# Kernel optimization log

Hardware: AMD Instinct MI355X
Metric: run time of the kernel (lower is better)

The kernel has to match this reference:

```python
import jax, jax.numpy as jnp
import numpy as np

EMBED_DIM = 512
NUM_HEADS = 8
HEAD_DIM = EMBED_DIM // NUM_HEADS


def setup_inputs() -> dict:
    key = jax.random.key(0)
    ks = jax.random.split(key, 5)
    B, N, D = 2, 4096, EMBED_DIM
    s_in = 1.0 / np.sqrt(D)
    x = jax.random.normal(ks[0], (B, N, D), dtype=jnp.float32)
    qkv_w = jax.random.uniform(ks[1], (3 * D, D), dtype=jnp.float32, minval=-s_in, maxval=s_in)
    qkv_b = jax.random.uniform(ks[2], (3 * D,), dtype=jnp.float32, minval=-s_in, maxval=s_in)
    out_w = jax.random.uniform(ks[3], (D, D), dtype=jnp.float32, minval=-s_in, maxval=s_in)
    out_b = jax.random.uniform(ks[4], (D,), dtype=jnp.float32, minval=-s_in, maxval=s_in)
    return {"x": x, "qkv_w": qkv_w, "qkv_b": qkv_b, "out_w": out_w, "out_b": out_b}


def reference(x, qkv_w, qkv_b, out_w, out_b):
    B, N, D = x.shape
    H, Hd = NUM_HEADS, HEAD_DIM
    # qkv projection: [B,N,3D] -> [3,B,H,N,Hd]
    qkv = x @ qkv_w.T + qkv_b
    qkv = qkv.reshape(B, N, 3, H, Hd).transpose(2, 0, 3, 1, 4)
    q, k, v = qkv[0], qkv[1], qkv[2]
    scale = 1.0 / jnp.sqrt(jnp.asarray(Hd, dtype=x.dtype))
    scores = jnp.einsum("bhnd,bhmd->bhnm", q, k) * scale  # [B,H,N,N]
    weights = jax.nn.softmax(scores, axis=-1)
    out = jnp.einsum("bhnm,bhmd->bhnd", weights, v)  # [B,H,N,Hd]
    out = out.transpose(0, 2, 1, 3).reshape(B, N, D)
    return out @ out_w.T + out_b
```

## Files before the change

### kernel.cpp

```cpp
#include <hip/hip_runtime.h>

typedef __attribute__((ext_vector_type(8))) short short8;
typedef __attribute__((ext_vector_type(4))) float f32x4;
typedef __attribute__((ext_vector_type(16))) float f32x16;
typedef unsigned short u16;
typedef unsigned int u32;

#define SCQ 0.18033688011112042f

__device__ __forceinline__ u16 f2b(float f) {
  unsigned u = __builtin_bit_cast(unsigned, f);
  u += 0x7FFFu + ((u >> 16) & 1u);
  return (u16)(u >> 16);
}

__device__ __forceinline__ u32 cvtpk(float a, float b) {
  u32 r;
  asm("v_cvt_pk_bf16_f32 %0, %1, %2" : "=v"(r) : "v"(a), "v"(b));
  return r;
}

__global__ __launch_bounds__(256) void convert_k(
    const float* __restrict__ x, const float* __restrict__ w1, const float* __restrict__ w2,
    u16* __restrict__ xb, u16* __restrict__ w1b, u16* __restrict__ w2b) {
  const int NXv = (8192 * 512) / 4;
  const int NW1v = (1536 * 512) / 4;
  const int NW2v = (512 * 512) / 4;
  int i = blockIdx.x * 256 + threadIdx.x;
  const float4* src;
  u16* dst;
  int j;
  float scale = 1.0f;
  if (i < NXv) {
    src = (const float4*)x; dst = xb; j = i;
  } else if (i < NXv + NW1v) {
    j = i - NXv; src = (const float4*)w1; dst = w1b;
    if (j < (512 * 512) / 4) scale = SCQ;
  } else {
    j = i - NXv - NW1v;
    if (j >= NW2v) return;
    src = (const float4*)w2; dst = w2b;
  }
  float4 v = src[j];
  ushort4 o;
  o.x = f2b(v.x * scale); o.y = f2b(v.y * scale);
  o.z = f2b(v.z * scale); o.w = f2b(v.w * scale);
  *reinterpret_cast<ushort4*>(dst + (size_t)j * 4) = o;
}

__global__ __launch_bounds__(256) void qkv_gemm(
    const u16* __restrict__ Ab, const u16* __restrict__ Bw, const float* __restrict__ bias,
    u16* __restrict__ Qd, u16* __restrict__ Kd, u16* __restrict__ Vtd) {
  const int m0 = blockIdx.x * 128, n0 = blockIdx.y * 64;
  const int tid = threadIdx.x, wave = tid >> 6, lane = tid & 63;
  const int g = lane >> 4, lr = lane & 15;
  const int wm = (wave >> 1) * 64, wn = (wave & 1) * 32;
  __shared__ alignas(16) u16 Al[128][72];
  __shared__ alignas(16) u16 Bl[64][72];

  f32x4 acc[4][2];
#pragma unroll
  for (int mf = 0; mf < 4; ++mf)
#pragma unroll
    for (int nf = 0; nf < 2; ++nf)
#pragma unroll
      for (int r = 0; r < 4; ++r) acc[mf][nf][r] = 0.0f;

  const int rr = tid >> 3, cc = tid & 7;
  for (int k0 = 0; k0 < 512; k0 += 64) {
    __syncthreads();
#pragma unroll
    for (int it = 0; it < 4; ++it)
      *reinterpret_cast<short8*>(&Al[rr + it * 32][cc * 8]) =
          *reinterpret_cast<const short8*>(Ab + (size_t)(m0 + rr + it * 32) * 512 + k0 + cc * 8);
#pragma unroll
    for (int it = 0; it < 2; ++it)
      *reinterpret_cast<short8*>(&Bl[rr + it * 32][cc * 8]) =
          *reinterpret_cast<const short8*>(Bw + (size_t)(n0 + rr + it * 32) * 512 + k0 + cc * 8);
    __syncthreads();
#pragma unroll
    for (int kb = 0; kb < 2; ++kb) {
      short8 bf[2], af[4];
#pragma unroll
      for (int nf = 0; nf < 2; ++nf)
        bf[nf] = *reinterpret_cast<const short8*>(&Bl[wn + nf * 16 + lr][kb * 32 + g * 8]);
#pragma unroll
      for (int mf = 0; mf < 4; ++mf)
        af[mf] = *reinterpret_cast<const short8*>(&Al[wm + mf * 16 + lr][kb * 32 + g * 8]);
#pragma unroll
      for (int mf = 0; mf < 4; ++mf)
#pragma unroll
        for (int nf = 0; nf < 2; ++nf)
          acc[mf][nf] = __builtin_amdgcn_mfma_f32_16x16x32_bf16(af[mf], bf[nf], acc[mf][nf], 0, 0, 0);
    }
  }
#pragma unroll
  for (int mf = 0; mf < 4; ++mf)
#pragma unroll
    for (int nf = 0; nf < 2; ++nf)
#pragma unroll
      for (int r = 0; r < 4; ++r) {
        int row = m0 + wm + mf * 16 + g * 4 + r;
        int col = n0 + wn + nf * 16 + lr;
        float bv = bias[col];
        if (col < 512) bv *= SCQ;
        u16 val = f2b(acc[mf][nf][r] + bv);
        int which = col >> 9, dcol = col & 511;
        int h = dcol >> 6, hd = dcol & 63;
        int b = row >> 12, n = row & 4095;
        size_t hb = (size_t)(b * 8 + h);
        if (which == 0)      Qd[(hb * 4096 + n) * 64 + hd] = val;
        else if (which == 1) Kd[(hb * 4096 + n) * 64 + hd] = val;
        else                 Vtd[(hb * 64 + hd) * 4096 + n] = val;
      }
}

__global__ __launch_bounds__(256, 2) void attn2(
    const u16* __restrict__ Qd, const u16* __restrict__ Kd, const u16* __restrict__ Vtd,
    float* __restrict__ Op, float* __restrict__ Lp) {
  int f = blockIdx.x + (blockIdx.y << 4) + (blockIdx.z << 8);
  int xcd = f & 7, slot = f >> 3;
  int bh = (xcd << 1) + (slot >> 5);
  int rem = slot & 31;
  int half = rem >> 4;
  int qb = rem & 15;

  const int tid = threadIdx.x, wave = tid >> 6, lane = tid & 63;
  const int hi = lane >> 5, lq = lane & 31;

  const u16* Qh = Qd + (size_t)bh * (4096 * 64);
  const u16* Kh = Kd + (size_t)bh * (4096 * 64);
  const u16* Vh = Vtd + (size_t)bh * (64 * 4096);
  float* Oh = Op + (size_t)half * (8192 * 512);
  float* Lh = Lp + (size_t)half * (16 * 4096);

  __shared__ alignas(16) u16 Kl[2][64 * 64];

  const int qrow_base = qb * 256 + wave * 64;

  short8 qf[2][4];
#pragma unroll
  for (int qt = 0; qt < 2; ++qt)
#pragma unroll
    for (int s = 0; s < 4; ++s)
      qf[qt][s] = *reinterpret_cast<const short8*>(
          Qh + (size_t)(qrow_base + qt * 32 + lq) * 64 + s * 16 + hi * 8);

  f32x16 acc[2][2];
#pragma unroll
  for (int qt = 0; qt < 2; ++qt)
#pragma unroll
    for (int dt = 0; dt < 2; ++dt)
#pragma unroll
      for (int i = 0; i < 16; ++i) acc[qt][dt][i] = 0.0f;

  float lrun[2] = {0.0f, 0.0f};

  const int kv0 = half * 2048;
  const int g0 = tid, g1 = tid + 256;
  const int sr0 = g0 >> 3, sc0 = g0 & 7;
  const int sr1 = g1 >> 3, sc1 = g1 & 7;

  {
    short8 t0 = *reinterpret_cast<const short8*>(Kh + (size_t)(kv0 + sr0) * 64 + sc0 * 8);
    short8 t1 = *reinterpret_cast<const short8*>(Kh + (size_t)(kv0 + sr1) * 64 + sc1 * 8);
    *reinterpret_cast<short8*>(&Kl[0][sr0 * 64 + ((sc0 ^ (sr0 & 7)) << 3)]) = t0;
    *reinterpret_cast<short8*>(&Kl[0][sr1 * 64 + ((sc1 ^ (sr1 & 7)) << 3)]) = t1;
  }
  __syncthreads();

#pragma unroll 1
  for (int kt = 0; kt < 32; ++kt) {
    const int cur = kt & 1;
    const int kbase = kv0 + kt * 64;
    short8 t0, t1;
    const bool pf = (kt + 1 < 32);
    if (pf) {
      t0 = *reinterpret_cast<const short8*>(Kh + (size_t)(kbase + 64 + sr0) * 64 + sc0 * 8);
      t1 = *reinterpret_cast<const short8*>(Kh + (size_t)(kbase + 64 + sr1) * 64 + sc1 * 8);
    }

    f32x16 st[2][2];
#pragma unroll
    for (int qt = 0; qt < 2; ++qt)
#pragma unroll
      for (int krt = 0; krt < 2; ++krt)
#pragma unroll
        for (int i = 0; i < 16; ++i) st[qt][krt][i] = 0.0f;

#pragma unroll
    for (int s = 0; s < 4; ++s) {
      const int ch = ((2 * s + hi) ^ (lq & 7)) << 3;
      short8 kf0 = *reinterpret_cast<const short8*>(&Kl[cur][lq * 64 + ch]);
      short8 kf1 = *reinterpret_cast<const short8*>(&Kl[cur][(32 + lq) * 64 + ch]);
      st[0][0] = __builtin_amdgcn_mfma_f32_32x32x16_bf16(kf0, qf[0][s], st[0][0], 0, 0, 0);
      st[0][1] = __builtin_amdgcn_mfma_f32_32x32x16_bf16(kf1, qf[0][s], st[0][1], 0, 0, 0);
      st[1][0] = __builtin_amdgcn_mfma_f32_32x32x16_bf16(kf0, qf[1][s], st[1][0], 0, 0, 0);
      st[1][1] = __builtin_amdgcn_mfma_f32_32x32x16_bf16(kf1, qf[1][s], st[1][1], 0, 0, 0);
    }

    short8 vf[4][2];
#pragma unroll
    for (int ks = 0; ks < 4; ++ks)
#pragma unroll
      for (int dt = 0; dt < 2; ++dt)
        vf[ks][dt] = *reinterpret_cast<const short8*>(
            Vh + (size_t)(dt * 32 + lq) * 4096 + kbase + ks * 16 + hi * 8);

    short8 pb[2][4];
#pragma unroll
    for (int qt = 0; qt < 2; ++qt) {
      float p[32];
#pragma unroll
      for (int i = 0; i < 16; ++i) p[i] = exp2f(st[qt][0][i]);
#pragma unroll
      for (int i = 0; i < 16; ++i) p[16 + i] = exp2f(st[qt][1][i]);
      float a0 = 0.f, a1 = 0.f, a2 = 0.f, a3 = 0.f;
#pragma unroll
      for (int i = 0; i < 32; i += 4) {
        a0 += p[i]; a1 += p[i + 1]; a2 += p[i + 2]; a3 += p[i + 3];
      }
      lrun[qt] += (a0 + a1) + (a2 + a3);
#pragma unroll
      for (int ks = 0; ks < 4; ++ks) {
        u32 wa = cvtpk(p[8 * ks + 0], p[8 * ks + 1]);
        u32 wb = cvtpk(p[8 * ks + 4], p[8 * ks + 5]);
        u32 wc = cvtpk(p[8 * ks + 2], p[8 * ks + 3]);
        u32 wd = cvtpk(p[8 * ks + 6], p[8 * ks + 7]);
        asm volatile("v_permlane32_swap_b32 %0, %1" : "+v"(wa), "+v"(wb));
        asm volatile("v_permlane32_swap_b32 %0, %1" : "+v"(wc), "+v"(wd));
        int4 wv;
        wv.x = (int)wa; wv.y = (int)wc; wv.z = (int)wb; wv.w = (int)wd;
        pb[qt][ks] = __builtin_bit_cast(short8, wv);
      }
    }

#pragma unroll
    for (int ks = 0; ks < 4; ++ks) {
      acc[0][0] = __builtin_amdgcn_mfma_f32_32x32x16_bf16(vf[ks][0], pb[0][ks], acc[0][0], 0, 0, 0);
      acc[0][1] = __builtin_amdgcn_mfma_f32_32x32x16_bf16(vf[ks][1], pb[0][ks], acc[0][1], 0, 0, 0);
      acc[1][0] = __builtin_amdgcn_mfma_f32_32x32x16_bf16(vf[ks][0], pb[1][ks], acc[1][0], 0, 0, 0);
      acc[1][1] = __builtin_amdgcn_mfma_f32_32x32x16_bf16(vf[ks][1], pb[1][ks], acc[1][1], 0, 0, 0);
    }

    if (pf) {
      *reinterpret_cast<short8*>(&Kl[cur ^ 1][sr0 * 64 + ((sc0 ^ (sr0 & 7)) << 3)]) = t0;
      *reinterpret_cast<short8*>(&Kl[cur ^ 1][sr1 * 64 + ((sc1 ^ (sr1 & 7)) << 3)]) = t1;
    }
    __syncthreads();
  }

  const int b = bh >> 3, h = bh & 7;
#pragma unroll
  for (int qt = 0; qt < 2; ++qt) {
    const int qn = qrow_base + qt * 32 + lq;
    const size_t rowoff = ((size_t)(b * 4096 + qn)) * 512 + h * 64;
#pragma unroll
    for (int dt = 0; dt < 2; ++dt)
#pragma unroll
      for (int t = 0; t < 4; ++t) {
        f32x4 v4;
        v4[0] = acc[qt][dt][4 * t + 0];
        v4[1] = acc[qt][dt][4 * t + 1];
        v4[2] = acc[qt][dt][4 * t + 2];
        v4[3] = acc[qt][dt][4 * t + 3];
        *reinterpret_cast<f32x4*>(Oh + rowoff + dt * 32 + t * 8 + hi * 4) = v4;
      }
    float lt = lrun[qt] + __shfl_xor(lrun[qt], 32);
    if (hi == 0) Lh[(bh << 12) + qn] = lt;
  }
}

__global__ __launch_bounds__(256) void combine_k(
    const float* __restrict__ O0, const float* __restrict__ O1,
    const float* __restrict__ L0, const float* __restrict__ L1,
    u16* __restrict__ attnb) {
  int idx = blockIdx.x * 256 + threadIdx.x;
  int row = idx >> 7, c4 = idx & 127;
  int b = row >> 12, n = row & 4095, h = c4 >> 4;
  int li = (((b << 3) + h) << 12) + n;
  float l = L0[li] + L1[li];
  float inv = 1.0f / l;
  float4 o0 = reinterpret_cast<const float4*>(O0)[idx];
  float4 o1 = reinterpret_cast<const float4*>(O1)[idx];
  ushort4 o;
  o.x = f2b((o0.x + o1.x) * inv);
  o.y = f2b((o0.y + o1.y) * inv);
  o.z = f2b((o0.z + o1.z) * inv);
  o.w = f2b((o0.w + o1.w) * inv);
  *reinterpret_cast<ushort4*>(attnb + (size_t)idx * 4) = o;
}

__global__ __launch_bounds__(256) void out_gemm(
    const u16* __restrict__ Ab, const u16* __restrict__ Bw, const float* __restrict__ bias,
    float* __restrict__ out) {
  const int m0 = blockIdx.x * 128, n0 = blockIdx.y * 64;
  const int tid = threadIdx.x, wave = tid >> 6, lane = tid & 63;
  const int g = lane >> 4, lr = lane & 15;
  const int wm = (wave >> 1) * 64, wn = (wave & 1) * 32;
  __shared__ alignas(16) u16 Al[128][72];
  __shared__ alignas(16) u16 Bl[64][72];

  f32x4 acc[4][2];
#pragma unroll
  for (int mf = 0; mf < 4; ++mf)
#pragma unroll
    for (int nf = 0; nf < 2; ++nf)
#pragma unroll
      for (int r = 0; r < 4; ++r) acc[mf][nf][r] = 0.0f;

  const int rr = tid >> 3, cc = tid & 7;
  for (int k0 = 0; k0 < 512; k0 += 64) {
    __syncthreads();
#pragma unroll
    for (int it = 0; it < 4; ++it)
      *reinterpret_cast<short8*>(&Al[rr + it * 32][cc * 8]) =
          *reinterpret_cast<const short8*>(Ab + (size_t)(m0 + rr + it * 32) * 512 + k0 + cc * 8);
#pragma unroll
    for (int it = 0; it < 2; ++it)
      *reinterpret_cast<short8*>(&Bl[rr + it * 32][cc * 8]) =
          *reinterpret_cast<const short8*>(Bw + (size_t)(n0 + rr + it * 32) * 512 + k0 + cc * 8);
    __syncthreads();
#pragma unroll
    for (int kb = 0; kb < 2; ++kb) {
      short8 bf[2], af[4];
#pragma unroll
      for (int nf = 0; nf < 2; ++nf)
        bf[nf] = *reinterpret_cast<const short8*>(&Bl[wn + nf * 16 + lr][kb * 32 + g * 8]);
#pragma unroll
      for (int mf = 0; mf < 4; ++mf)
        af[mf] = *reinterpret_cast<const short8*>(&Al[wm + mf * 16 + lr][kb * 32 + g * 8]);
#pragma unroll
      for (int mf = 0; mf < 4; ++mf)
#pragma unroll
        for (int nf = 0; nf < 2; ++nf)
          acc[mf][nf] = __builtin_amdgcn_mfma_f32_16x16x32_bf16(af[mf], bf[nf], acc[mf][nf], 0, 0, 0);
    }
  }
#pragma unroll
  for (int mf = 0; mf < 4; ++mf)
#pragma unroll
    for (int nf = 0; nf < 2; ++nf)
#pragma unroll
      for (int r = 0; r < 4; ++r) {
        int row = m0 + wm + mf * 16 + g * 4 + r;
        int col = n0 + wn + nf * 16 + lr;
        out[(size_t)row * 512 + col] = acc[mf][nf][r] + bias[col];
      }
}

extern "C" void kernel_launch(void* const* d_in, const int* in_sizes, int n_in,
                              void* d_out, int out_size, void* d_ws, size_t ws_size,
                              hipStream_t stream) {
  const float* x = (const float*)d_in[0];
  const float* qkv_w = (const float*)d_in[1];
  const float* qkv_b = (const float*)d_in[2];
  const float* out_w = (const float*)d_in[3];
  const float* out_b = (const float*)d_in[4];
  float* out = (float*)d_out;

  char* ws = (char*)d_ws;
  u16* xb    = (u16*)(ws + 0);
  u16* w1b   = (u16*)(ws + 8388608);
  u16* w2b   = (u16*)(ws + 9961472);
  u16* Qd    = (u16*)(ws + 10485760);
  u16* Kd    = (u16*)(ws + 18874368);
  u16* Vtd   = (u16*)(ws + 27262976);
  u16* attnb = (u16*)(ws + 35651584);
  float* Op  = (float*)(ws + 44040192);
  float* Lp  = (float*)(ws + 77594624);

  convert_k<<<5120, 256, 0, stream>>>(x, qkv_w, out_w, xb, w1b, w2b);
  qkv_gemm<<<dim3(64, 24), 256, 0, stream>>>(xb, w1b, qkv_b, Qd, Kd, Vtd);
  attn2<<<dim3(16, 16, 2), 256, 0, stream>>>(Qd, Kd, Vtd, Op, Lp);
  combine_k<<<4096, 256, 0, stream>>>(Op, Op + 8192 * 512, Lp, Lp + 16 * 4096, attnb);
  out_gemm<<<dim3(64, 8), 256, 0, stream>>>(attnb, w2b, out_b, out);
}
```

Baseline: 156.9 us.

## Split KV across waves within block and reduce partials in LDS, drop combine kernel

The attention kernel now gives each block 64 query rows and splits the key/value range across its four waves, 1024 keys each. Each wave reads K fragments straight from global memory instead of using a shared double-buffered tile, which removes the per-iteration block barrier. Partial outputs and row sums are reduced through LDS at the end, and the normalised bf16 result is written directly, removing the fp32 partial buffers and the separate combine kernel. The cost is K traffic no longer shared through LDS, a large LDS reduction buffer, and a launch bound of 4 blocks per SM that may limit registers.

```diff
diff --git a/kernel.cpp b/kernel.cpp
--- a/kernel.cpp
+++ b/kernel.cpp
@@ -115,15 +115,13 @@
       }
 }
 
-__global__ __launch_bounds__(256, 2) void attn2(
+__global__ __launch_bounds__(256, 4) void attn4(
     const u16* __restrict__ Qd, const u16* __restrict__ Kd, const u16* __restrict__ Vtd,
-    float* __restrict__ Op, float* __restrict__ Lp) {
-  int f = blockIdx.x + (blockIdx.y << 4) + (blockIdx.z << 8);
+    u16* __restrict__ attnb) {
+  int f = blockIdx.x;
   int xcd = f & 7, slot = f >> 3;
-  int bh = (xcd << 1) + (slot >> 5);
-  int rem = slot & 31;
-  int half = rem >> 4;
-  int qb = rem & 15;
+  int bh = (xcd << 1) + (slot >> 6);
+  int qb = slot & 63;
 
   const int tid = threadIdx.x, wave = tid >> 6, lane = tid & 63;
   const int hi = lane >> 5, lq = lane & 31;
@@ -131,12 +129,8 @@
   const u16* Qh = Qd + (size_t)bh * (4096 * 64);
   const u16* Kh = Kd + (size_t)bh * (4096 * 64);
   const u16* Vh = Vtd + (size_t)bh * (64 * 4096);
-  float* Oh = Op + (size_t)half * (8192 * 512);
-  float* Lh = Lp + (size_t)half * (16 * 4096);
-
-  __shared__ alignas(16) u16 Kl[2][64 * 64];
-
-  const int qrow_base = qb * 256 + wave * 64;
+
+  const int qrow_base = qb * 64;
 
   short8 qf[2][4];
 #pragma unroll
@@ -156,29 +150,19 @@
 
   float lrun[2] = {0.0f, 0.0f};
 
-  const int kv0 = half * 2048;
-  const int g0 = tid, g1 = tid + 256;
-  const int sr0 = g0 >> 3, sc0 = g0 & 7;
-  const int sr1 = g1 >> 3, sc1 = g1 & 7;
-
-  {
-    short8 t0 = *reinterpret_cast<const short8*>(Kh + (size_t)(kv0 + sr0) * 64 + sc0 * 8);
-    short8 t1 = *reinterpret_cast<const short8*>(Kh + (size_t)(kv0 + sr1) * 64 + sc1 * 8);
-    *reinterpret_cast<short8*>(&Kl[0][sr0 * 64 + ((sc0 ^ (sr0 & 7)) << 3)]) = t0;
-    *reinterpret_cast<short8*>(&Kl[0][sr1 * 64 + ((sc1 ^ (sr1 & 7)) << 3)]) = t1;
-  }
-  __syncthreads();
+  const int kv0 = wave * 1024;
 
 #pragma unroll 1
-  for (int kt = 0; kt < 32; ++kt) {
-    const int cur = kt & 1;
+  for (int kt = 0; kt < 16; ++kt) {
     const int kbase = kv0 + kt * 64;
-    short8 t0, t1;
-    const bool pf = (kt + 1 < 32);
-    if (pf) {
-      t0 = *reinterpret_cast<const short8*>(Kh + (size_t)(kbase + 64 + sr0) * 64 + sc0 * 8);
-      t1 = *reinterpret_cast<const short8*>(Kh + (size_t)(kbase + 64 + sr1) * 64 + sc1 * 8);
-    }
+
+    short8 kf[2][4];
+#pragma unroll
+    for (int krt = 0; krt < 2; ++krt)
+#pragma unroll
+      for (int s = 0; s < 4; ++s)
+        kf[krt][s] = *reinterpret_cast<const short8*>(
+            Kh + (size_t)(kbase + krt * 32 + lq) * 64 + s * 16 + hi * 8);
 
     f32x16 st[2][2];
 #pragma unroll
@@ -187,16 +171,12 @@
       for (int krt = 0; krt < 2; ++krt)
 #pragma unroll
         for (int i = 0; i < 16; ++i) st[qt][krt][i] = 0.0f;
-
 #pragma unroll
     for (int s = 0; s < 4; ++s) {
-      const int ch = ((2 * s + hi) ^ (lq & 7)) << 3;
-      short8 kf0 = *reinterpret_cast<const short8*>(&Kl[cur][lq * 64 + ch]);
-      short8 kf1 = *reinterpret_cast<const short8*>(&Kl[cur][(32 + lq) * 64 + ch]);
-      st[0][0] = __builtin_amdgcn_mfma_f32_32x32x16_bf16(kf0, qf[0][s], st[0][0], 0, 0, 0);
-      st[0][1] = __builtin_amdgcn_mfma_f32_32x32x16_bf16(kf1, qf[0][s], st[0][1], 0, 0, 0);
-      st[1][0] = __builtin_amdgcn_mfma_f32_32x32x16_bf16(kf0, qf[1][s], st[1][0], 0, 0, 0);
-      st[1][1] = __builtin_amdgcn_mfma_f32_32x32x16_bf16(kf1, qf[1][s], st[1][1], 0, 0, 0);
+      st[0][0] = __builtin_amdgcn_mfma_f32_32x32x16_bf16(kf[0][s], qf[0][s], st[0][0], 0, 0, 0);
+      st[0][1] = __builtin_amdgcn_mfma_f32_32x32x16_bf16(kf[1][s], qf[0][s], st[0][1], 0, 0, 0);
+      st[1][0] = __builtin_amdgcn_mfma_f32_32x32x16_bf16(kf[0][s], qf[1][s], st[1][0], 0, 0, 0);
+      st[1][1] = __builtin_amdgcn_mfma_f32_32x32x16_bf16(kf[1][s], qf[1][s], st[1][1], 0, 0, 0);
     }
 
     short8 vf[4][2];
@@ -242,53 +222,45 @@
       acc[1][0] = __builtin_amdgcn_mfma_f32_32x32x16_bf16(vf[ks][0], pb[1][ks], acc[1][0], 0, 0, 0);
       acc[1][1] = __builtin_amdgcn_mfma_f32_32x32x16_bf16(vf[ks][1], pb[1][ks], acc[1][1], 0, 0, 0);
     }
-
-    if (pf) {
-      *reinterpret_cast<short8*>(&Kl[cur ^ 1][sr0 * 64 + ((sc0 ^ (sr0 & 7)) << 3)]) = t0;
-      *reinterpret_cast<short8*>(&Kl[cur ^ 1][sr1 * 64 + ((sc1 ^ (sr1 & 7)) << 3)]) = t1;
-    }
-    __syncthreads();
-  }
-
-  const int b = bh >> 3, h = bh & 7;
+  }
+
+  __shared__ float Pl[4][2][2][16][64];
+  __shared__ float Ll[4][2][64];
 #pragma unroll
   for (int qt = 0; qt < 2; ++qt) {
-    const int qn = qrow_base + qt * 32 + lq;
-    const size_t rowoff = ((size_t)(b * 4096 + qn)) * 512 + h * 64;
 #pragma unroll
     for (int dt = 0; dt < 2; ++dt)
 #pragma unroll
-      for (int t = 0; t < 4; ++t) {
-        f32x4 v4;
-        v4[0] = acc[qt][dt][4 * t + 0];
-        v4[1] = acc[qt][dt][4 * t + 1];
-        v4[2] = acc[qt][dt][4 * t + 2];
-        v4[3] = acc[qt][dt][4 * t + 3];
-        *reinterpret_cast<f32x4*>(Oh + rowoff + dt * 32 + t * 8 + hi * 4) = v4;
-      }
-    float lt = lrun[qt] + __shfl_xor(lrun[qt], 32);
-    if (hi == 0) Lh[(bh << 12) + qn] = lt;
-  }
-}
-
-__global__ __launch_bounds__(256) void combine_k(
-    const float* __restrict__ O0, const float* __restrict__ O1,
-    const float* __restrict__ L0, const float* __restrict__ L1,
-    u16* __restrict__ attnb) {
-  int idx = blockIdx.x * 256 + threadIdx.x;
-  int row = idx >> 7, c4 = idx & 127;
-  int b = row >> 12, n = row & 4095, h = c4 >> 4;
-  int li = (((b << 3) + h) << 12) + n;
-  float l = L0[li] + L1[li];
-  float inv = 1.0f / l;
-  float4 o0 = reinterpret_cast<const float4*>(O0)[idx];
-  float4 o1 = reinterpret_cast<const float4*>(O1)[idx];
-  ushort4 o;
-  o.x = f2b((o0.x + o1.x) * inv);
-  o.y = f2b((o0.y + o1.y) * inv);
-  o.z = f2b((o0.z + o1.z) * inv);
-  o.w = f2b((o0.w + o1.w) * inv);
-  *reinterpret_cast<ushort4*>(attnb + (size_t)idx * 4) = o;
+      for (int i = 0; i < 16; ++i) Pl[wave][qt][dt][i][lane] = acc[qt][dt][i];
+    Ll[wave][qt][lane] = lrun[qt];
+  }
+  __syncthreads();
+
+  {
+    const int qt = wave >> 1, dt = wave & 1;
+    float v[16];
+#pragma unroll
+    for (int i = 0; i < 16; ++i)
+      v[i] = (Pl[0][qt][dt][i][lane] + Pl[1][qt][dt][i][lane]) +
+             (Pl[2][qt][dt][i][lane] + Pl[3][qt][dt][i][lane]);
+    float l = 0.0f;
+#pragma unroll
+    for (int s = 0; s < 4; ++s) l += Ll[s][qt][lq] + Ll[s][qt][32 + lq];
+    const float inv = 1.0f / l;
+
+    const int b = bh >> 3, h = bh & 7;
+    const int qrow = qrow_base + qt * 32 + lq;
+    u16* dst = attnb + (size_t)(b * 4096 + qrow) * 512 + h * 64 + dt * 32;
+#pragma unroll
+    for (int t = 0; t < 4; ++t) {
+      ushort4 o;
+      o.x = f2b(v[4 * t + 0] * inv);
+      o.y = f2b(v[4 * t + 1] * inv);
+      o.z = f2b(v[4 * t + 2] * inv);
+      o.w = f2b(v[4 * t + 3] * inv);
+      *reinterpret_cast<ushort4*>(dst + 8 * t + 4 * hi) = o;
+    }
+  }
 }
 
 __global__ __launch_bounds__(256) void out_gemm(
@@ -367,12 +339,9 @@
   u16* Kd    = (u16*)(ws + 18874368);
   u16* Vtd   = (u16*)(ws + 27262976);
   u16* attnb = (u16*)(ws + 35651584);
-  float* Op  = (float*)(ws + 44040192);
-  float* Lp  = (float*)(ws + 77594624);
 
   convert_k<<<5120, 256, 0, stream>>>(x, qkv_w, out_w, xb, w1b, w2b);
   qkv_gemm<<<dim3(64, 24), 256, 0, stream>>>(xb, w1b, qkv_b, Qd, Kd, Vtd);
-  attn2<<<dim3(16, 16, 2), 256, 0, stream>>>(Qd, Kd, Vtd, Op, Lp);
-  combine_k<<<4096, 256, 0, stream>>>(Op, Op + 8192 * 512, Lp, Lp + 16 * 4096, attnb);
+  attn4<<<1024, 256, 0, stream>>>(Qd, Kd, Vtd, attnb);
   out_gemm<<<dim3(64, 8), 256, 0, stream>>>(attnb, w2b, out_b, out);
 }
```

After: 192.6 us. 22.8% more time.
